# Kernel tuning notes

Measured on AMD Instinct MI355X. Metric: run time of the kernel, lower is better.

The kernel has to match this reference:

```python
import jax, jax.numpy as jnp
import numpy as np

N = 50000
E = 1600000
IN_C, H1, H2 = 512, 512, 256
N_CLASSES = 40
CENTER_NUM = 8
D_CAT = 2 * H2  # 512


def setup_inputs() -> dict:
    key = jax.random.key(0)
    ks = jax.random.split(key, 9)
    x = jax.random.normal(ks[0], (N, IN_C), dtype=jnp.float32)
    edge_index = jax.random.randint(ks[1], (2, E), 0, N, dtype=jnp.int64)
    s1 = 1.0 / np.sqrt(IN_C)
    s2 = 1.0 / np.sqrt(H1)
    sp = 1.0 / np.sqrt(D_CAT)
    W1 = jax.random.uniform(ks[2], (IN_C, H1), jnp.float32, -s1, s1)
    b1 = jnp.zeros((H1,), jnp.float32)
    W2 = jax.random.uniform(ks[3], (H1, H2), jnp.float32, -s2, s2)
    b2 = jnp.zeros((H2,), jnp.float32)
    Wp = jax.random.uniform(ks[4], (CENTER_NUM, D_CAT), jnp.float32, -sp, sp)   # interior_prototype weight [C, D]
    We = jax.random.uniform(ks[5], (CENTER_NUM, N_CLASSES, D_CAT), jnp.float32, -sp, sp)  # border prototypes
    return {"x": x, "edge_index": edge_index, "W1": W1, "b1": b1, "W2": W2, "b2": b2, "Wp": Wp, "We": We}


def _gcn_conv(x, W, b, src, dst, n):
    # PyG GCNConv: h = xW; out[i] = sum_j norm_ij h[j] + b, with self-loops,
    # norm_ij = deg_i^{-1/2} deg_j^{-1/2}, deg includes self-loop.
    h = x @ W
    ones = jnp.ones(src.shape[0], x.dtype)
    deg = jax.ops.segment_sum(ones, dst, num_segments=n) + 1.0
    dinv = deg ** -0.5
    norm = dinv[src] * dinv[dst]
    agg = jax.ops.segment_sum(h[src] * norm[:, None], dst, num_segments=n)
    agg = agg + h * (dinv * dinv)[:, None]  # self-loop term
    return agg + b


def _mean_aggr(x, src, dst, n):
    # PyG default message x_j with aggr='mean' (custom message_func kwarg is ignored by PyG)
    cnt = jax.ops.segment_sum(jnp.ones(src.shape[0], x.dtype), dst, num_segments=n)
    s = jax.ops.segment_sum(x[src], dst, num_segments=n)
    return s / jnp.maximum(cnt, 1.0)[:, None]


def reference(x, edge_index, W1, b1, W2, b2, Wp, We):
    src, dst = edge_index[0], edge_index[1]
    n = x.shape[0]
    h = jax.nn.relu(_gcn_conv(x, W1, b1, src, dst, n))
    h = _gcn_conv(h, W2, b2, src, dst, n)
    neighbor = _mean_aggr(h, src, dst, n)
    xc = jnp.concatenate([h, neighbor], axis=1)  # [N, 2*H2]
    scores = xc @ Wp.T                            # [N, C]
    idx = jnp.argmax(scores, axis=1)              # [N]
    # all-expert logits then per-node select (same math as masked per-cluster linear)
    all_out = jnp.einsum('nd,ckd->nck', xc, We)   # [N, C, n_classes]
    out = jnp.take_along_axis(all_out, idx[:, None, None], axis=1)[:, 0, :]
    return out, xc
```

## Files before the change

### kernel.cpp

```cpp
#include <hip/hip_runtime.h>
#include <hip/hip_bf16.h>
#include <hip/hip_fp16.h>
#include <cstdint>
#include <cstddef>


using short8 = __attribute__((ext_vector_type(8))) short;
using half8  = __attribute__((ext_vector_type(8))) _Float16;
using f32x4  = __attribute__((ext_vector_type(4))) float;

#define GLB_AS __attribute__((address_space(1)))
#define LDS_AS __attribute__((address_space(3)))

__device__ inline void unpack_fma(int v, float w, float* a) {
    a[0] = fmaf(w, (float)(char)(v),       a[0]);
    a[1] = fmaf(w, (float)(char)(v >> 8),  a[1]);
    a[2] = fmaf(w, (float)(char)(v >> 16), a[2]);
    a[3] = fmaf(w, (float)(v >> 24),       a[3]);
}

__global__ __launch_bounds__(256) void prep_kernel(
    const float* __restrict__ x, char* __restrict__ xq, float* __restrict__ scale,
    const float* __restrict__ W1, __half* __restrict__ W1T,
    const float* __restrict__ W2, __half* __restrict__ W2T,
    const float* __restrict__ We, __half* __restrict__ We_h,
    int* __restrict__ bcur, int* __restrict__ ecur,
    int n, int nbuck, int cap) {
    const int t = threadIdx.x;
    int b = blockIdx.x;
    const int BXQ = (n + 3) / 4;
    const int BW1 = (512 * 512) / 256;
    const int BW2 = (512 * 256) / 256;
    const int BWe = (8 * 40 * 512) / 256;
    if (b < BXQ) {
        const int node = b * 4 + (t >> 6);
        const int lane = t & 63;
        if (node < n) {
            const float* row = x + (size_t)node * 512;
            const float4 v0 = *(const float4*)&row[lane * 8];
            const float4 v1 = *(const float4*)&row[lane * 8 + 4];
            float m = fmaxf(fmaxf(fmaxf(fabsf(v0.x), fabsf(v0.y)), fmaxf(fabsf(v0.z), fabsf(v0.w))),
                            fmaxf(fmaxf(fabsf(v1.x), fabsf(v1.y)), fmaxf(fabsf(v1.z), fabsf(v1.w))));
#pragma unroll
            for (int off = 32; off; off >>= 1) m = fmaxf(m, __shfl_xor(m, off));
            m = fmaxf(m, 1e-30f);
            const float qs = 127.f / m;
            int q0 = __float2int_rn(v0.x * qs), q1 = __float2int_rn(v0.y * qs);
            int q2 = __float2int_rn(v0.z * qs), q3 = __float2int_rn(v0.w * qs);
            int q4 = __float2int_rn(v1.x * qs), q5 = __float2int_rn(v1.y * qs);
            int q6 = __float2int_rn(v1.z * qs), q7 = __float2int_rn(v1.w * qs);
            uint2 pk;
            pk.x = (q0 & 0xff) | ((q1 & 0xff) << 8) | ((q2 & 0xff) << 16) | ((q3 & 0xff) << 24);
            pk.y = (q4 & 0xff) | ((q5 & 0xff) << 8) | ((q6 & 0xff) << 16) | ((q7 & 0xff) << 24);
            *(uint2*)&xq[(size_t)node * 512 + lane * 8] = pk;
            if (lane == 0) scale[node] = m / 127.f;
        }
        return;
    }
    b -= BXQ;
    if (b < BW1) {
        const int gid = b * 256 + t;
        const int k = gid >> 9, nn = gid & 511;
        W1T[(size_t)nn * 512 + k] = __float2half(W1[gid]);
        return;
    }
    b -= BW1;
    if (b < BW2) {
        const int gid = b * 256 + t;
        const int k = gid >> 8, nn = gid & 255;
        W2T[(size_t)nn * 512 + k] = __float2half(W2[gid]);
        return;
    }
    b -= BW2;
    if (b < BWe) {
        const int gid = b * 256 + t;
        We_h[gid] = __float2half(We[gid]);
        return;
    }
    if (t < nbuck) bcur[t] = t * cap;
    if (t < 8) ecur[t] = 0;
}

__global__ __launch_bounds__(256) void bucketA_kernel(const int* __restrict__ src,
                                                      const int* __restrict__ dst,
                                                      int* __restrict__ bcur,
                                                      uint32_t* __restrict__ ebuf, int e) {
    __shared__ uint32_t sbuf[4096];
    __shared__ int h[128], gb[128], c2[128];
    const int t = threadIdx.x;
    if (t < 128) { h[t] = 0; c2[t] = 0; }
    __syncthreads();
    const int base = blockIdx.x * 4096;
    const int m = min(4096, e - base);
    for (int j = t; j < m; j += 256) {
        const int s = src[base + j];
        const int d = dst[base + j];
        sbuf[j] = ((uint32_t)s << 16) | (uint32_t)d;
        atomicAdd(&h[d >> 9], 1);
    }
    __syncthreads();
    if (t < 128 && h[t] > 0) gb[t] = atomicAdd(&bcur[t], h[t]);
    __syncthreads();
    for (int j = t; j < m; j += 256) {
        const uint32_t pf = sbuf[j];
        const int b = (int)((pf & 0xFFFFu) >> 9);
        const int r = atomicAdd(&c2[b], 1);
        ebuf[gb[b] + r] = pf;
    }
}

__global__ __launch_bounds__(256) void bucketB_kernel(const uint32_t* __restrict__ ebuf,
                                                      const int* __restrict__ bcur,
                                                      const float* __restrict__ scale,
                                                      int* __restrict__ offsets,
                                                      int* __restrict__ counts,
                                                      float* __restrict__ dinv,
                                                      float* __restrict__ dsc,
                                                      int* __restrict__ ssrc,
                                                      int n, int cap) {
    __shared__ int h[512];
    __shared__ int lofs[512];
    __shared__ int sc[256];
    const int t = threadIdx.x;
    const int b = blockIdx.x;
    const int nbase = b * 512;
    const int nb = min(512, n - nbase);
    h[t] = 0; h[t + 256] = 0;
    __syncthreads();
    const int ebeg = b * cap;
    const int ecount = bcur[b] - ebeg;
    for (int j = t; j < ecount; j += 256)
        atomicAdd(&h[ebuf[ebeg + j] & 511u], 1);
    __syncthreads();
    const int pair = h[2 * t] + h[2 * t + 1];
    sc[t] = pair;
    __syncthreads();
    for (int off = 1; off < 256; off <<= 1) {
        const int u = (t >= off) ? sc[t - off] : 0;
        __syncthreads();
        sc[t] += u;
        __syncthreads();
    }
    const int pbase = sc[t] - pair;
    lofs[2 * t] = pbase;
    lofs[2 * t + 1] = pbase + h[2 * t];
    __syncthreads();
    for (int j = t; j < nb; j += 256) {
        const int cnt = h[j];
        const float dv = rsqrtf((float)cnt + 1.0f);
        offsets[nbase + j] = ebeg + lofs[j];
        counts[nbase + j] = cnt;
        dinv[nbase + j] = dv;
        dsc[nbase + j] = dv * scale[nbase + j];
    }
    __syncthreads();
    lofs[2 * t] += ebeg;
    lofs[2 * t + 1] += ebeg;
    __syncthreads();
    for (int j = t; j < ecount; j += 256) {
        const uint32_t pf = ebuf[ebeg + j];
        const int d = (int)(pf & 511u);
        const int s = (int)(pf >> 16);
        const int pos = atomicAdd(&lofs[d], 1);
        ssrc[pos] = s;
    }
}

__global__ __launch_bounds__(256) void agg512_kernel(const char* __restrict__ xq,
                                                     const int* __restrict__ ssrc,
                                                     const int* __restrict__ offsets,
                                                     const int* __restrict__ counts,
                                                     const float* __restrict__ dinv,
                                                     const float* __restrict__ dsc,
                                                     __half* __restrict__ A16, int n) {
    const int lane = threadIdx.x & 63;
    const int node = (blockIdx.x * blockDim.x + threadIdx.x) >> 6;
    if (node >= n) return;
    const int beg = offsets[node];
    const int end = beg + counts[node];
    const float di = dinv[node];
    const int half = lane >> 5;
    const int hl = lane & 31;
    float acc[16];
#pragma unroll
    for (int j = 0; j < 16; ++j) acc[j] = 0.f;

    for (int b0 = beg; b0 < end; b0 += 64) {
        const int idx = b0 + lane;
        const int sl = (idx < end) ? ssrc[idx] : 0;
        const float wl = (idx < end) ? di * dsc[sl] : 0.f;
        const int m = min(64, end - b0);
#pragma unroll 8
        for (int kp = 0; kp < m; kp += 2) {
            const int k = kp + half;
            const int s = __shfl(sl, k);
            const float w = __shfl(wl, k);
            const int4 raw = *(const int4*)&xq[(size_t)s * 512 + hl * 16];
            unpack_fma(raw.x, w, &acc[0]);
            unpack_fma(raw.y, w, &acc[4]);
            unpack_fma(raw.z, w, &acc[8]);
            unpack_fma(raw.w, w, &acc[12]);
        }
    }
#pragma unroll
    for (int j = 0; j < 16; ++j) acc[j] += __shfl(acc[j], hl + 32);

    if (half == 0) {
        const float w = di * dsc[node];
        const int4 raw = *(const int4*)&xq[(size_t)node * 512 + hl * 16];
        unpack_fma(raw.x, w, &acc[0]);
        unpack_fma(raw.y, w, &acc[4]);
        unpack_fma(raw.z, w, &acc[8]);
        unpack_fma(raw.w, w, &acc[12]);
        float4 pk0, pk1;
        *(__half2*)&pk0.x = __floats2half2_rn(acc[0], acc[1]);
        *(__half2*)&pk0.y = __floats2half2_rn(acc[2], acc[3]);
        *(__half2*)&pk0.z = __floats2half2_rn(acc[4], acc[5]);
        *(__half2*)&pk0.w = __floats2half2_rn(acc[6], acc[7]);
        *(__half2*)&pk1.x = __floats2half2_rn(acc[8], acc[9]);
        *(__half2*)&pk1.y = __floats2half2_rn(acc[10], acc[11]);
        *(__half2*)&pk1.z = __floats2half2_rn(acc[12], acc[13]);
        *(__half2*)&pk1.w = __floats2half2_rn(acc[14], acc[15]);
        *(float4*)&A16[(size_t)node * 512 + hl * 16] = pk0;
        *(float4*)&A16[(size_t)node * 512 + hl * 16 + 8] = pk1;
    }
}

__global__ __launch_bounds__(256) void tquant_kernel(const __half* __restrict__ t16,
                                                     const float* __restrict__ dinv,
                                                     char* __restrict__ tq,
                                                     float* __restrict__ dts, int n) {
    const int lane = threadIdx.x & 63;
    const int node = (blockIdx.x * blockDim.x + threadIdx.x) >> 6;
    if (node >= n) return;
    const float2 raw = *(const float2*)&t16[(size_t)node * 256 + lane * 4];
    const float2 f0 = __half22float2(*(const __half2*)&raw.x);
    const float2 f1 = __half22float2(*(const __half2*)&raw.y);
    float m = fmaxf(fmaxf(fabsf(f0.x), fabsf(f0.y)), fmaxf(fabsf(f1.x), fabsf(f1.y)));
#pragma unroll
    for (int off = 32; off; off >>= 1) m = fmaxf(m, __shfl_xor(m, off));
    m = fmaxf(m, 1e-30f);
    const float qs = 127.f / m;
    const int q0 = __float2int_rn(f0.x * qs), q1 = __float2int_rn(f0.y * qs);
    const int q2 = __float2int_rn(f1.x * qs), q3 = __float2int_rn(f1.y * qs);
    const uint32_t pk = (q0 & 0xff) | ((q1 & 0xff) << 8) | ((q2 & 0xff) << 16) | ((q3 & 0xff) << 24);
    *(uint32_t*)&tq[(size_t)node * 256 + lane * 4] = pk;
    if (lane == 0) dts[node] = dinv[node] * (m / 127.f);
}

__global__ __launch_bounds__(256) void agg256_kernel(const char* __restrict__ tq,
                                                     const int* __restrict__ ssrc,
                                                     const int* __restrict__ offsets,
                                                     const int* __restrict__ counts,
                                                     const float* __restrict__ dinv,
                                                     const float* __restrict__ dts,
                                                     const float* __restrict__ bias,
                                                     float* __restrict__ xc,
                                                     __half* __restrict__ h2h,
                                                     char* __restrict__ hq8,
                                                     float* __restrict__ hsc, int n) {
    const int lane = threadIdx.x & 63;
    const int node = (blockIdx.x * blockDim.x + threadIdx.x) >> 6;
    if (node >= n) return;
    const int beg = offsets[node];
    const int end = beg + counts[node];
    const float di = dinv[node];
    const int q = lane >> 4;
    const int ql = lane & 15;
    float acc[16];
#pragma unroll
    for (int j = 0; j < 16; ++j) acc[j] = 0.f;

    for (int b0 = beg; b0 < end; b0 += 64) {
        const int idx = b0 + lane;
        const int sl = (idx < end) ? ssrc[idx] : 0;
        const float wl = (idx < end) ? di * dts[sl] : 0.f;
        const int m = min(64, end - b0);
#pragma unroll 4
        for (int kp = 0; kp < m; kp += 4) {
            const int k = kp + q;
            const int s = __shfl(sl, k);
            const float w = __shfl(wl, k);
            const int4 raw = *(const int4*)&tq[(size_t)s * 256 + ql * 16];
            unpack_fma(raw.x, w, &acc[0]);
            unpack_fma(raw.y, w, &acc[4]);
            unpack_fma(raw.z, w, &acc[8]);
            unpack_fma(raw.w, w, &acc[12]);
        }
    }
#pragma unroll
    for (int j = 0; j < 16; ++j) acc[j] += __shfl(acc[j], lane + 32);
#pragma unroll
    for (int j = 0; j < 16; ++j) acc[j] += __shfl(acc[j], lane + 16);

    if (q == 0) {
        const float w = di * dts[node];
        const int4 raw = *(const int4*)&tq[(size_t)node * 256 + ql * 16];
        unpack_fma(raw.x, w, &acc[0]);
        unpack_fma(raw.y, w, &acc[4]);
        unpack_fma(raw.z, w, &acc[8]);
        unpack_fma(raw.w, w, &acc[12]);
#pragma unroll
        for (int i = 0; i < 4; ++i) {
            const float4 bv = *(const float4*)&bias[ql * 16 + i * 4];
            acc[i * 4 + 0] += bv.x; acc[i * 4 + 1] += bv.y;
            acc[i * 4 + 2] += bv.z; acc[i * 4 + 3] += bv.w;
        }
#pragma unroll
        for (int i = 0; i < 4; ++i)
            *(float4*)&xc[(size_t)node * 512 + ql * 16 + i * 4] =
                make_float4(acc[i * 4 + 0], acc[i * 4 + 1], acc[i * 4 + 2], acc[i * 4 + 3]);
        float4 pk0, pk1;
        *(__half2*)&pk0.x = __floats2half2_rn(acc[0], acc[1]);
        *(__half2*)&pk0.y = __floats2half2_rn(acc[2], acc[3]);
        *(__half2*)&pk0.z = __floats2half2_rn(acc[4], acc[5]);
        *(__half2*)&pk0.w = __floats2half2_rn(acc[6], acc[7]);
        *(__half2*)&pk1.x = __floats2half2_rn(acc[8], acc[9]);
        *(__half2*)&pk1.y = __floats2half2_rn(acc[10], acc[11]);
        *(__half2*)&pk1.z = __floats2half2_rn(acc[12], acc[13]);
        *(__half2*)&pk1.w = __floats2half2_rn(acc[14], acc[15]);
        *(float4*)&h2h[(size_t)node * 256 + ql * 16] = pk0;
        *(float4*)&h2h[(size_t)node * 256 + ql * 16 + 8] = pk1;
        float am = 0.f;
#pragma unroll
        for (int j = 0; j < 16; ++j) am = fmaxf(am, fabsf(acc[j]));
#pragma unroll
        for (int off = 1; off < 16; off <<= 1) am = fmaxf(am, __shfl_xor(am, off));
        am = fmaxf(am, 1e-30f);
        const float qs = 127.f / am;
        uint32_t pk[4];
#pragma unroll
        for (int i = 0; i < 4; ++i) {
            const int a0 = __float2int_rn(acc[i * 4 + 0] * qs);
            const int a1 = __float2int_rn(acc[i * 4 + 1] * qs);
            const int a2 = __float2int_rn(acc[i * 4 + 2] * qs);
            const int a3 = __float2int_rn(acc[i * 4 + 3] * qs);
            pk[i] = (a0 & 0xff) | ((a1 & 0xff) << 8) | ((a2 & 0xff) << 16) | ((a3 & 0xff) << 24);
        }
        *(int4*)&hq8[(size_t)node * 256 + ql * 16] = *(int4*)pk;
        if (ql == 0) hsc[node] = am / 127.f;
    }
}

template <int EPI>
__global__ __launch_bounds__(256) void gemm_f16_kernel(
    const __half* __restrict__ A, const __half* __restrict__ WT,
    const float* __restrict__ bias, __half* __restrict__ C,
    int M, int N, int K, int ldc) {
    __shared__ ushort smem[2 * 4096];
    const int tid = threadIdx.x;
    const int lane = tid & 63;
    const int w = tid >> 6;
    const int wr = w >> 1, wc = w & 1;
    const int bm = blockIdx.y * 128;
    const int bn = blockIdx.x * 128;

    f32x4 acc[4][4];
#pragma unroll
    for (int i = 0; i < 4; ++i)
#pragma unroll
        for (int j = 0; j < 4; ++j) acc[i][j] = f32x4{0.f, 0.f, 0.f, 0.f};

    for (int k0 = 0; k0 < K; k0 += 32) {
        __syncthreads();
#pragma unroll
        for (int i = 0; i < 4; ++i) {
            const int q = w * 4 + i;
            const bool isA = q < 8;
            const int seg = (isA ? q : q - 8) * 64 + lane;
            const int row = seg >> 2;
            const int kc = (seg & 3) * 8;
            int grow = (isA ? bm : bn) + row;
            grow = min(grow, (isA ? M : N) - 1);
            const ushort* g = (const ushort*)(isA ? A : WT) + (size_t)grow * K + k0 + kc;
            __builtin_amdgcn_global_load_lds((const GLB_AS void*)g,
                                             (LDS_AS void*)(smem + q * 512), 16, 0, 0);
        }
        __syncthreads();

        const int koff = (lane >> 4) * 8;
        const int rsel = lane & 15;
        half8 a[4], b[4];
#pragma unroll
        for (int f = 0; f < 4; ++f) {
            const int ar = wr * 64 + f * 16 + rsel;
            a[f] = __builtin_bit_cast(half8, *(const short8*)&smem[ar * 32 + koff]);
            const int bc = wc * 64 + f * 16 + rsel;
            b[f] = __builtin_bit_cast(half8, *(const short8*)&smem[4096 + bc * 32 + koff]);
        }
#pragma unroll
        for (int i = 0; i < 4; ++i)
#pragma unroll
            for (int j = 0; j < 4; ++j)
                acc[i][j] = __builtin_amdgcn_mfma_f32_16x16x32_f16(a[i], b[j], acc[i][j], 0, 0, 0);
    }

    const int crow0 = wr * 64 + (lane >> 4) * 4;
    const int ccol0 = wc * 64 + (lane & 15);
#pragma unroll
    for (int f = 0; f < 4; ++f) {
#pragma unroll
        for (int g = 0; g < 4; ++g) {
            const int colg = bn + ccol0 + g * 16;
            float bv = 0.f;
            if constexpr (EPI == 1) bv = bias[colg];
#pragma unroll
            for (int j = 0; j < 4; ++j) {
                const int rowg = bm + crow0 + f * 16 + j;
                if (rowg >= M) continue;
                float v = acc[f][g][j];
                if constexpr (EPI == 1) v = fmaxf(v + bv, 0.f);
                C[(size_t)rowg * ldc + colg] = __float2half(v);
            }
        }
    }
}

__global__ __launch_bounds__(256) void mean_score_kernel(const int* __restrict__ ssrc,
                                                         const int* __restrict__ offsets,
                                                         const int* __restrict__ counts,
                                                         const float* __restrict__ Wp,
                                                         const char* __restrict__ hq8,
                                                         const float* __restrict__ hsc,
                                                         float* __restrict__ xc,
                                                         __half* __restrict__ mh,
                                                         int* __restrict__ bidx, int n) {
    __shared__ float lds_f[4][512];
    const int lane = threadIdx.x & 63;
    const int w = threadIdx.x >> 6;
    const int node = (blockIdx.x * blockDim.x + threadIdx.x) >> 6;
    if (node >= n) return;
    const int beg = offsets[node];
    const int cnt = counts[node];
    const int end = beg + cnt;
    const int c0 = lane * 4;
    const int q = lane >> 4;
    const int ql = lane & 15;

    float acc[16];
#pragma unroll
    for (int j = 0; j < 16; ++j) acc[j] = 0.f;
    for (int b0 = beg; b0 < end; b0 += 64) {
        const int idx = b0 + lane;
        const int sl = (idx < end) ? ssrc[idx] : 0;
        const float wl = (idx < end) ? hsc[sl] : 0.f;
        const int m = min(64, end - b0);
#pragma unroll 4
        for (int kp = 0; kp < m; kp += 4) {
            const int k = kp + q;
            const int s = __shfl(sl, k);
            const float ww = __shfl(wl, k);
            const int4 raw = *(const int4*)&hq8[(size_t)s * 256 + ql * 16];
            unpack_fma(raw.x, ww, &acc[0]);
            unpack_fma(raw.y, ww, &acc[4]);
            unpack_fma(raw.z, ww, &acc[8]);
            unpack_fma(raw.w, ww, &acc[12]);
        }
    }
#pragma unroll
    for (int j = 0; j < 16; ++j) acc[j] += __shfl(acc[j], lane + 32);
#pragma unroll
    for (int j = 0; j < 16; ++j) acc[j] += __shfl(acc[j], lane + 16);

    const float inv = 1.f / fmaxf((float)cnt, 1.f);
    if (q == 0) {
#pragma unroll
        for (int j = 0; j < 16; ++j) acc[j] *= inv;
#pragma unroll
        for (int i = 0; i < 4; ++i) {
            const float4 v = make_float4(acc[i * 4 + 0], acc[i * 4 + 1], acc[i * 4 + 2], acc[i * 4 + 3]);
            *(float4*)&xc[(size_t)node * 512 + 256 + ql * 16 + i * 4] = v;
            *(float4*)&lds_f[w][256 + ql * 16 + i * 4] = v;
        }
        float4 pk0, pk1;
        *(__half2*)&pk0.x = __floats2half2_rn(acc[0], acc[1]);
        *(__half2*)&pk0.y = __floats2half2_rn(acc[2], acc[3]);
        *(__half2*)&pk0.z = __floats2half2_rn(acc[4], acc[5]);
        *(__half2*)&pk0.w = __floats2half2_rn(acc[6], acc[7]);
        *(__half2*)&pk1.x = __floats2half2_rn(acc[8], acc[9]);
        *(__half2*)&pk1.y = __floats2half2_rn(acc[10], acc[11]);
        *(__half2*)&pk1.z = __floats2half2_rn(acc[12], acc[13]);
        *(__half2*)&pk1.w = __floats2half2_rn(acc[14], acc[15]);
        *(float4*)&mh[(size_t)node * 256 + ql * 16] = pk0;
        *(float4*)&mh[(size_t)node * 256 + ql * 16 + 8] = pk1;
    }
    const float4 a = *(const float4*)&xc[(size_t)node * 512 + c0];
    *(float4*)&lds_f[w][c0] = a;

    const int r = lane & 15;
    const int quad = lane >> 4;

    float av[32];
#pragma unroll
    for (int i = 0; i < 8; ++i) {
        const int jj = (i + r) & 7;
        *(float4*)&av[i * 4] = *(const float4*)&lds_f[w][r * 32 + jj * 4];
    }

    float s0, s1;
#pragma unroll
    for (int t = 0; t < 2; ++t) {
        const int c = t * 4 + quad;
        const float* wp = &Wp[c * 512 + r * 32];
        float p = 0.f;
#pragma unroll
        for (int i = 0; i < 8; ++i) {
            const int jj = (i + r) & 7;
            const float4 wv = *(const float4*)&wp[jj * 4];
            p = fmaf(av[i * 4 + 0], wv.x, p);
            p = fmaf(av[i * 4 + 1], wv.y, p);
            p = fmaf(av[i * 4 + 2], wv.z, p);
            p = fmaf(av[i * 4 + 3], wv.w, p);
        }
        p += __shfl_xor(p, 1); p += __shfl_xor(p, 2);
        p += __shfl_xor(p, 4); p += __shfl_xor(p, 8);
        if (t == 0) s0 = p; else s1 = p;
    }
    float best = -3.0e38f;
    int be = 0;
#pragma unroll
    for (int c = 0; c < 8; ++c) {
        const float v = __shfl((c < 4) ? s0 : s1, (c & 3) * 16);
        if (v > best) { best = v; be = c; }
    }
    if (lane == 0) bidx[node] = be;
}

__global__ __launch_bounds__(256) void bucket_scatter_kernel(const int* __restrict__ bidx,
                                                             int* __restrict__ cursor,
                                                             int* __restrict__ elist, int n) {
    __shared__ int h[8], base[8], c2[8];
    const int t = threadIdx.x;
    if (t < 8) { h[t] = 0; c2[t] = 0; }
    __syncthreads();
    const int i = blockIdx.x * 256 + t;
    int b = 0;
    if (i < n) {
        b = bidx[i];
        atomicAdd(&h[b], 1);
    }
    __syncthreads();
    if (t < 8) base[t] = (h[t] > 0) ? atomicAdd(&cursor[t], h[t]) : 0;
    __syncthreads();
    if (i < n) {
        const int r = atomicAdd(&c2[b], 1);
        elist[(size_t)b * n + base[b] + r] = i;
    }
}

__global__ __launch_bounds__(256) void expert_gemm_kernel(
    const int* __restrict__ elist, const int* __restrict__ ecnt,
    const __half* __restrict__ h2h, const __half* __restrict__ mh,
    const __half* __restrict__ We_h, float* __restrict__ out, int n) {
    const int e = blockIdx.x;
    const int cnt = ecnt[e];
    const int base = blockIdx.y * 128;
    if (base >= cnt) return;
    __shared__ __half Bs[40][520];
    const int tid = threadIdx.x;
#pragma unroll
    for (int i = 0; i < 10; ++i) {
        const int seg = tid + i * 256;
        const int br = seg >> 6;
        const int bc = (seg & 63) * 8;
        *(float4*)&Bs[br][bc] = *(const float4*)&We_h[((size_t)e * 40 + br) * 512 + bc];
    }
    __syncthreads();

    const int w = tid >> 6, lane = tid & 63;
    const int rsel = lane & 15, koff = (lane >> 4) * 8;
    const int grow0 = base + w * 32 + rsel;
    const int grow1 = grow0 + 16;
    const int i0 = elist[(size_t)e * n + min(grow0, cnt - 1)];
    const int i1 = elist[(size_t)e * n + min(grow1, cnt - 1)];

    f32x4 acc[2][3];
#pragma unroll
    for (int mf = 0; mf < 2; ++mf)
#pragma unroll
        for (int nf = 0; nf < 3; ++nf) acc[mf][nf] = f32x4{0.f, 0.f, 0.f, 0.f};

#pragma unroll
    for (int ks = 0; ks < 16; ++ks) {
        const int k0 = ks * 32 + koff;
        const __half* s0 = (k0 < 256) ? &h2h[(size_t)i0 * 256 + k0] : &mh[(size_t)i0 * 256 + (k0 - 256)];
        const __half* s1 = (k0 < 256) ? &h2h[(size_t)i1 * 256 + k0] : &mh[(size_t)i1 * 256 + (k0 - 256)];
        const half8 a0 = __builtin_bit_cast(half8, *(const short8*)s0);
        const half8 a1 = __builtin_bit_cast(half8, *(const short8*)s1);
#pragma unroll
        for (int nf = 0; nf < 3; ++nf) {
            const int brow = min(nf * 16 + rsel, 39);
            const half8 b = __builtin_bit_cast(half8, *(const short8*)&Bs[brow][ks * 32 + koff]);
            acc[0][nf] = __builtin_amdgcn_mfma_f32_16x16x32_f16(a0, b, acc[0][nf], 0, 0, 0);
            acc[1][nf] = __builtin_amdgcn_mfma_f32_16x16x32_f16(a1, b, acc[1][nf], 0, 0, 0);
        }
    }

    const int crow = (lane >> 4) * 4;
    const int ccol = lane & 15;
#pragma unroll
    for (int mf = 0; mf < 2; ++mf) {
#pragma unroll
        for (int nf = 0; nf < 3; ++nf) {
            const int col = nf * 16 + ccol;
            if (col >= 40) continue;
#pragma unroll
            for (int j = 0; j < 4; ++j) {
                const int gr = base + w * 32 + mf * 16 + crow + j;
                if (gr >= cnt) continue;
                const int node = elist[(size_t)e * n + gr];
                out[(size_t)node * 40 + col] = acc[mf][nf][j];
            }
        }
    }
}

extern "C" void kernel_launch(void* const* d_in, const int* in_sizes, int n_in,
                              void* d_out, int out_size, void* d_ws, size_t ws_size,
                              hipStream_t stream) {
    const float* x  = (const float*)d_in[0];
    const int*  edge = (const int*)d_in[1];
    const float* W1 = (const float*)d_in[2];
    const float* b1 = (const float*)d_in[3];
    const float* W2 = (const float*)d_in[4];
    const float* b2 = (const float*)d_in[5];
    const float* Wp = (const float*)d_in[6];
    const float* We = (const float*)d_in[7];

    const int n = in_sizes[0] / 512;
    const int e = in_sizes[1] / 2;
    const int* src = edge;
    const int* dst = edge + e;

    const int nbuck = (n + 511) / 512;
    const int cap = 20480;

    char* ws = (char*)d_ws;
    __half* A16 = (__half*)ws;
    __half* t16 = (__half*)ws;
    __half* mh  = (__half*)ws;
    char* p = ws + (size_t)n * 512 * 2;
    __half* h1 = (__half*)p;
    __half* h2h = (__half*)p;
    p += (size_t)n * 512 * 2;
    char* xq  = p; p += (size_t)n * 512;
    char* tq8 = p; p += (size_t)n * 256;
    char* hq8 = p; p += (size_t)n * 256;
    __half* W1T = (__half*)p; p += 512 * 512 * 2;
    __half* W2T = (__half*)p; p += 256 * 512 * 2;
    __half* We_h = (__half*)p; p += 8 * 40 * 512 * 2;
    auto align16 = [](size_t v) { return (v + 15) & ~(size_t)15; };
    float* scale = (float*)p;   p += align16((size_t)n * 4);
    float* dinv = (float*)p;    p += align16((size_t)n * 4);
    float* dsc = (float*)p;     p += align16((size_t)n * 4);
    float* dts = (float*)p;     p += align16((size_t)n * 4);
    float* hsc = (float*)p;     p += align16((size_t)n * 4);
    int* counts = (int*)p;      p += align16((size_t)n * 4);
    int* offsets = (int*)p;     p += align16((size_t)n * 4);
    int* bidx = (int*)p;        p += align16((size_t)n * 4);
    int* bcur = (int*)p;        p += align16((size_t)nbuck * 4);
    int* ecur = (int*)p;        p += align16((size_t)8 * 4);
    int* elist = (int*)p;       p += align16((size_t)8 * n * 4);
    uint32_t* ebuf = (uint32_t*)p; p += align16((size_t)nbuck * cap * 4);
    int* ssrc = (int*)p;

    float* out = (float*)d_out;
    float* xc = (float*)d_out + (size_t)n * 40;

    const int prep_blocks = (n + 3) / 4 + (512 * 512) / 256 +
                            (512 * 256) / 256 + (8 * 40 * 512) / 256 + 1;
    prep_kernel<<<prep_blocks, 256, 0, stream>>>(x, xq, scale, W1, W1T, W2, W2T, We, We_h,
                                                 bcur, ecur, n, nbuck, cap);

    bucketA_kernel<<<(e + 4095) / 4096, 256, 0, stream>>>(src, dst, bcur, ebuf, e);
    bucketB_kernel<<<nbuck, 256, 0, stream>>>(ebuf, bcur, scale, offsets, counts, dinv, dsc,
                                              ssrc, n, cap);

    const int waves_grid = (n * 64 + 255) / 256;
    agg512_kernel<<<waves_grid, 256, 0, stream>>>(xq, ssrc, offsets, counts, dinv, dsc, A16, n);
    dim3 g1(512 / 128, (n + 127) / 128);
    gemm_f16_kernel<1><<<g1, 256, 0, stream>>>(A16, W1T, b1, h1, n, 512, 512, 512);

    dim3 g2(256 / 128, (n + 127) / 128);
    gemm_f16_kernel<0><<<g2, 256, 0, stream>>>(h1, W2T, nullptr, t16, n, 256, 512, 256);
    tquant_kernel<<<waves_grid, 256, 0, stream>>>(t16, dinv, tq8, dts, n);

    agg256_kernel<<<waves_grid, 256, 0, stream>>>(tq8, ssrc, offsets, counts, dinv, dts, b2,
                                                  xc, h2h, hq8, hsc, n);

    mean_score_kernel<<<waves_grid, 256, 0, stream>>>(ssrc, offsets, counts, Wp, hq8, hsc,
                                                      xc, mh, bidx, n);

    bucket_scatter_kernel<<<(n + 255) / 256, 256, 0, stream>>>(bidx, ecur, elist, n);

    dim3 ge(8, (n + 127) / 128);
    expert_gemm_kernel<<<ge, 256, 0, stream>>>(elist, ecur, h2h, mh, We_h, out, n);
}
```

Before: 557.9 us.

## Switch int8 activations to offset-uint8 and feed the expert GEMM from 8-bit data

```diff
diff --git a/kernel.cpp b/kernel.cpp
--- a/kernel.cpp
+++ b/kernel.cpp
@@ -8,19 +8,34 @@
 using short8 = __attribute__((ext_vector_type(8))) short;
 using half8  = __attribute__((ext_vector_type(8))) _Float16;
 using f32x4  = __attribute__((ext_vector_type(4))) float;
+typedef unsigned char uchar;
 
 #define GLB_AS __attribute__((address_space(1)))
 #define LDS_AS __attribute__((address_space(3)))
 
-__device__ inline void unpack_fma(int v, float w, float* a) {
-    a[0] = fmaf(w, (float)(char)(v),       a[0]);
-    a[1] = fmaf(w, (float)(char)(v >> 8),  a[1]);
-    a[2] = fmaf(w, (float)(char)(v >> 16), a[2]);
-    a[3] = fmaf(w, (float)(v >> 24),       a[3]);
+__device__ inline void unpack_fma_u(uint32_t v, float w, float* a) {
+    a[0] = fmaf(w, (float)(v & 0xffu),         a[0]);
+    a[1] = fmaf(w, (float)((v >> 8) & 0xffu),  a[1]);
+    a[2] = fmaf(w, (float)((v >> 16) & 0xffu), a[2]);
+    a[3] = fmaf(w, (float)(v >> 24),           a[3]);
+}
+
+__device__ inline half8 dequant8(uint2 raw, float s) {
+    const float off = -128.f * s;
+    half8 r;
+    r[0] = (_Float16)fmaf(s, (float)(raw.x & 0xffu), off);
+    r[1] = (_Float16)fmaf(s, (float)((raw.x >> 8) & 0xffu), off);
+    r[2] = (_Float16)fmaf(s, (float)((raw.x >> 16) & 0xffu), off);
+    r[3] = (_Float16)fmaf(s, (float)(raw.x >> 24), off);
+    r[4] = (_Float16)fmaf(s, (float)(raw.y & 0xffu), off);
+    r[5] = (_Float16)fmaf(s, (float)((raw.y >> 8) & 0xffu), off);
+    r[6] = (_Float16)fmaf(s, (float)((raw.y >> 16) & 0xffu), off);
+    r[7] = (_Float16)fmaf(s, (float)(raw.y >> 24), off);
+    return r;
 }
 
 __global__ __launch_bounds__(256) void prep_kernel(
-    const float* __restrict__ x, char* __restrict__ xq, float* __restrict__ scale,
+    const float* __restrict__ x, uchar* __restrict__ xq, float* __restrict__ scale,
     const float* __restrict__ W1, __half* __restrict__ W1T,
     const float* __restrict__ W2, __half* __restrict__ W2T,
     const float* __restrict__ We, __half* __restrict__ We_h,
@@ -45,13 +60,13 @@
             for (int off = 32; off; off >>= 1) m = fmaxf(m, __shfl_xor(m, off));
             m = fmaxf(m, 1e-30f);
             const float qs = 127.f / m;
-            int q0 = __float2int_rn(v0.x * qs), q1 = __float2int_rn(v0.y * qs);
-            int q2 = __float2int_rn(v0.z * qs), q3 = __float2int_rn(v0.w * qs);
-            int q4 = __float2int_rn(v1.x * qs), q5 = __float2int_rn(v1.y * qs);
-            int q6 = __float2int_rn(v1.z * qs), q7 = __float2int_rn(v1.w * qs);
+            const int q0 = __float2int_rn(v0.x * qs) + 128, q1 = __float2int_rn(v0.y * qs) + 128;
+            const int q2 = __float2int_rn(v0.z * qs) + 128, q3 = __float2int_rn(v0.w * qs) + 128;
+            const int q4 = __float2int_rn(v1.x * qs) + 128, q5 = __float2int_rn(v1.y * qs) + 128;
+            const int q6 = __float2int_rn(v1.z * qs) + 128, q7 = __float2int_rn(v1.w * qs) + 128;
             uint2 pk;
-            pk.x = (q0 & 0xff) | ((q1 & 0xff) << 8) | ((q2 & 0xff) << 16) | ((q3 & 0xff) << 24);
-            pk.y = (q4 & 0xff) | ((q5 & 0xff) << 8) | ((q6 & 0xff) << 16) | ((q7 & 0xff) << 24);
+            pk.x = q0 | (q1 << 8) | (q2 << 16) | (q3 << 24);
+            pk.y = q4 | (q5 << 8) | (q6 << 16) | (q7 << 24);
             *(uint2*)&xq[(size_t)node * 512 + lane * 8] = pk;
             if (lane == 0) scale[node] = m / 127.f;
         }
@@ -166,7 +181,7 @@
     }
 }
 
-__global__ __launch_bounds__(256) void agg512_kernel(const char* __restrict__ xq,
+__global__ __launch_bounds__(256) void agg512_kernel(const uchar* __restrict__ xq,
                                                      const int* __restrict__ ssrc,
                                                      const int* __restrict__ offsets,
                                                      const int* __restrict__ counts,
@@ -184,6 +199,7 @@
     float acc[16];
 #pragma unroll
     for (int j = 0; j < 16; ++j) acc[j] = 0.f;
+    float wsum = 0.f;
 
     for (int b0 = beg; b0 < end; b0 += 64) {
         const int idx = b0 + lane;
@@ -195,23 +211,28 @@
             const int k = kp + half;
             const int s = __shfl(sl, k);
             const float w = __shfl(wl, k);
-            const int4 raw = *(const int4*)&xq[(size_t)s * 512 + hl * 16];
-            unpack_fma(raw.x, w, &acc[0]);
-            unpack_fma(raw.y, w, &acc[4]);
-            unpack_fma(raw.z, w, &acc[8]);
-            unpack_fma(raw.w, w, &acc[12]);
+            wsum += w;
+            const uint4 raw = *(const uint4*)&xq[(size_t)s * 512 + hl * 16];
+            unpack_fma_u(raw.x, w, &acc[0]);
+            unpack_fma_u(raw.y, w, &acc[4]);
+            unpack_fma_u(raw.z, w, &acc[8]);
+            unpack_fma_u(raw.w, w, &acc[12]);
         }
     }
 #pragma unroll
     for (int j = 0; j < 16; ++j) acc[j] += __shfl(acc[j], hl + 32);
+    wsum += __shfl(wsum, hl + 32);
 
     if (half == 0) {
         const float w = di * dsc[node];
-        const int4 raw = *(const int4*)&xq[(size_t)node * 512 + hl * 16];
-        unpack_fma(raw.x, w, &acc[0]);
-        unpack_fma(raw.y, w, &acc[4]);
-        unpack_fma(raw.z, w, &acc[8]);
-        unpack_fma(raw.w, w, &acc[12]);
+        wsum += w;
+        const uint4 raw = *(const uint4*)&xq[(size_t)node * 512 + hl * 16];
+        unpack_fma_u(raw.x, w, &acc[0]);
+        unpack_fma_u(raw.y, w, &acc[4]);
+        unpack_fma_u(raw.z, w, &acc[8]);
+        unpack_fma_u(raw.w, w, &acc[12]);
+#pragma unroll
+        for (int j = 0; j < 16; ++j) acc[j] = fmaf(-128.f, wsum, acc[j]);
         float4 pk0, pk1;
         *(__half2*)&pk0.x = __floats2half2_rn(acc[0], acc[1]);
         *(__half2*)&pk0.y = __floats2half2_rn(acc[2], acc[3]);
@@ -228,7 +249,7 @@
 
 __global__ __launch_bounds__(256) void tquant_kernel(const __half* __restrict__ t16,
                                                      const float* __restrict__ dinv,
-                                                     char* __restrict__ tq,
+                                                     uchar* __restrict__ tq,
                                                      float* __restrict__ dts, int n) {
     const int lane = threadIdx.x & 63;
     const int node = (blockIdx.x * blockDim.x + threadIdx.x) >> 6;
@@ -241,14 +262,14 @@
     for (int off = 32; off; off >>= 1) m = fmaxf(m, __shfl_xor(m, off));
     m = fmaxf(m, 1e-30f);
     const float qs = 127.f / m;
-    const int q0 = __float2int_rn(f0.x * qs), q1 = __float2int_rn(f0.y * qs);
-    const int q2 = __float2int_rn(f1.x * qs), q3 = __float2int_rn(f1.y * qs);
-    const uint32_t pk = (q0 & 0xff) | ((q1 & 0xff) << 8) | ((q2 & 0xff) << 16) | ((q3 & 0xff) << 24);
+    const int q0 = __float2int_rn(f0.x * qs) + 128, q1 = __float2int_rn(f0.y * qs) + 128;
+    const int q2 = __float2int_rn(f1.x * qs) + 128, q3 = __float2int_rn(f1.y * qs) + 128;
+    const uint32_t pk = q0 | (q1 << 8) | (q2 << 16) | (q3 << 24);
     *(uint32_t*)&tq[(size_t)node * 256 + lane * 4] = pk;
     if (lane == 0) dts[node] = dinv[node] * (m / 127.f);
 }
 
-__global__ __launch_bounds__(256) void agg256_kernel(const char* __restrict__ tq,
+__global__ __launch_bounds__(256) void agg256_kernel(const uchar* __restrict__ tq,
                                                      const int* __restrict__ ssrc,
                                                      const int* __restrict__ offsets,
                                                      const int* __restrict__ counts,
@@ -256,8 +277,7 @@
                                                      const float* __restrict__ dts,
                                                      const float* __restrict__ bias,
                                                      float* __restrict__ xc,
-                                                     __half* __restrict__ h2h,
-                                                     char* __restrict__ hq8,
+                                                     uchar* __restrict__ hq8,
                                                      float* __restrict__ hsc, int n) {
     const int lane = threadIdx.x & 63;
     const int node = (blockIdx.x * blockDim.x + threadIdx.x) >> 6;
@@ -270,6 +290,7 @@
     float acc[16];
 #pragma unroll
     for (int j = 0; j < 16; ++j) acc[j] = 0.f;
+    float wsum = 0.f;
 
     for (int b0 = beg; b0 < end; b0 += 64) {
         const int idx = b0 + lane;
@@ -281,25 +302,31 @@
             const int k = kp + q;
             const int s = __shfl(sl, k);
             const float w = __shfl(wl, k);
-            const int4 raw = *(const int4*)&tq[(size_t)s * 256 + ql * 16];
-            unpack_fma(raw.x, w, &acc[0]);
-            unpack_fma(raw.y, w, &acc[4]);
-            unpack_fma(raw.z, w, &acc[8]);
-            unpack_fma(raw.w, w, &acc[12]);
+            wsum += w;
+            const uint4 raw = *(const uint4*)&tq[(size_t)s * 256 + ql * 16];
+            unpack_fma_u(raw.x, w, &acc[0]);
+            unpack_fma_u(raw.y, w, &acc[4]);
+            unpack_fma_u(raw.z, w, &acc[8]);
+            unpack_fma_u(raw.w, w, &acc[12]);
         }
     }
 #pragma unroll
     for (int j = 0; j < 16; ++j) acc[j] += __shfl(acc[j], lane + 32);
+    wsum += __shfl(wsum, lane + 32);
 #pragma unroll
     for (int j = 0; j < 16; ++j) acc[j] += __shfl(acc[j], lane + 16);
+    wsum += __shfl(wsum, lane + 16);
 
     if (q == 0) {
         const float w = di * dts[node];
-        const int4 raw = *(const int4*)&tq[(size_t)node * 256 + ql * 16];
-        unpack_fma(raw.x, w, &acc[0]);
-        unpack_fma(raw.y, w, &acc[4]);
-        unpack_fma(raw.z, w, &acc[8]);
-        unpack_fma(raw.w, w, &acc[12]);
+        wsum += w;
+        const uint4 raw = *(const uint4*)&tq[(size_t)node * 256 + ql * 16];
+        unpack_fma_u(raw.x, w, &acc[0]);
+        unpack_fma_u(raw.y, w, &acc[4]);
+        unpack_fma_u(raw.z, w, &acc[8]);
+        unpack_fma_u(raw.w, w, &acc[12]);
+#pragma unroll
+        for (int j = 0; j < 16; ++j) acc[j] = fmaf(-128.f, wsum, acc[j]);
 #pragma unroll
         for (int i = 0; i < 4; ++i) {
             const float4 bv = *(const float4*)&bias[ql * 16 + i * 4];
@@ -310,17 +337,6 @@
         for (int i = 0; i < 4; ++i)
             *(float4*)&xc[(size_t)node * 512 + ql * 16 + i * 4] =
                 make_float4(acc[i * 4 + 0], acc[i * 4 + 1], acc[i * 4 + 2], acc[i * 4 + 3]);
-        float4 pk0, pk1;
-        *(__half2*)&pk0.x = __floats2half2_rn(acc[0], acc[1]);
-        *(__half2*)&pk0.y = __floats2half2_rn(acc[2], acc[3]);
-        *(__half2*)&pk0.z = __floats2half2_rn(acc[4], acc[5]);
-        *(__half2*)&pk0.w = __floats2half2_rn(acc[6], acc[7]);
-        *(__half2*)&pk1.x = __floats2half2_rn(acc[8], acc[9]);
-        *(__half2*)&pk1.y = __floats2half2_rn(acc[10], acc[11]);
-        *(__half2*)&pk1.z = __floats2half2_rn(acc[12], acc[13]);
-        *(__half2*)&pk1.w = __floats2half2_rn(acc[14], acc[15]);
-        *(float4*)&h2h[(size_t)node * 256 + ql * 16] = pk0;
-        *(float4*)&h2h[(size_t)node * 256 + ql * 16 + 8] = pk1;
         float am = 0.f;
 #pragma unroll
         for (int j = 0; j < 16; ++j) am = fmaxf(am, fabsf(acc[j]));
@@ -331,13 +347,13 @@
         uint32_t pk[4];
 #pragma unroll
         for (int i = 0; i < 4; ++i) {
-            const int a0 = __float2int_rn(acc[i * 4 + 0] * qs);
-            const int a1 = __float2int_rn(acc[i * 4 + 1] * qs);
-            const int a2 = __float2int_rn(acc[i * 4 + 2] * qs);
-            const int a3 = __float2int_rn(acc[i * 4 + 3] * qs);
-            pk[i] = (a0 & 0xff) | ((a1 & 0xff) << 8) | ((a2 & 0xff) << 16) | ((a3 & 0xff) << 24);
-        }
-        *(int4*)&hq8[(size_t)node * 256 + ql * 16] = *(int4*)pk;
+            const int a0 = __float2int_rn(acc[i * 4 + 0] * qs) + 128;
+            const int a1 = __float2int_rn(acc[i * 4 + 1] * qs) + 128;
+            const int a2 = __float2int_rn(acc[i * 4 + 2] * qs) + 128;
+            const int a3 = __float2int_rn(acc[i * 4 + 3] * qs) + 128;
+            pk[i] = a0 | (a1 << 8) | (a2 << 16) | (a3 << 24);
+        }
+        *(uint4*)&hq8[(size_t)node * 256 + ql * 16] = *(uint4*)pk;
         if (ql == 0) hsc[node] = am / 127.f;
     }
 }
@@ -420,10 +436,11 @@
                                                          const int* __restrict__ offsets,
                                                          const int* __restrict__ counts,
                                                          const float* __restrict__ Wp,
-                                                         const char* __restrict__ hq8,
+                                                         const uchar* __restrict__ hq8,
                                                          const float* __restrict__ hsc,
                                                          float* __restrict__ xc,
-                                                         __half* __restrict__ mh,
+                                                         uchar* __restrict__ mq8,
+                                                         float* __restrict__ msc,
                                                          int* __restrict__ bidx, int n) {
     __shared__ float lds_f[4][512];
     const int lane = threadIdx.x & 63;
@@ -440,6 +457,7 @@
     float acc[16];
 #pragma unroll
     for (int j = 0; j < 16; ++j) acc[j] = 0.f;
+    float wsum = 0.f;
     for (int b0 = beg; b0 < end; b0 += 64) {
         const int idx = b0 + lane;
         const int sl = (idx < end) ? ssrc[idx] : 0;
@@ -450,39 +468,49 @@
             const int k = kp + q;
             const int s = __shfl(sl, k);
             const float ww = __shfl(wl, k);
-            const int4 raw = *(const int4*)&hq8[(size_t)s * 256 + ql * 16];
-            unpack_fma(raw.x, ww, &acc[0]);
-            unpack_fma(raw.y, ww, &acc[4]);
-            unpack_fma(raw.z, ww, &acc[8]);
-            unpack_fma(raw.w, ww, &acc[12]);
+            wsum += ww;
+            const uint4 raw = *(const uint4*)&hq8[(size_t)s * 256 + ql * 16];
+            unpack_fma_u(raw.x, ww, &acc[0]);
+            unpack_fma_u(raw.y, ww, &acc[4]);
+            unpack_fma_u(raw.z, ww, &acc[8]);
+            unpack_fma_u(raw.w, ww, &acc[12]);
         }
     }
 #pragma unroll
     for (int j = 0; j < 16; ++j) acc[j] += __shfl(acc[j], lane + 32);
+    wsum += __shfl(wsum, lane + 32);
 #pragma unroll
     for (int j = 0; j < 16; ++j) acc[j] += __shfl(acc[j], lane + 16);
+    wsum += __shfl(wsum, lane + 16);
 
     const float inv = 1.f / fmaxf((float)cnt, 1.f);
     if (q == 0) {
 #pragma unroll
-        for (int j = 0; j < 16; ++j) acc[j] *= inv;
+        for (int j = 0; j < 16; ++j) acc[j] = fmaf(-128.f, wsum, acc[j]) * inv;
 #pragma unroll
         for (int i = 0; i < 4; ++i) {
             const float4 v = make_float4(acc[i * 4 + 0], acc[i * 4 + 1], acc[i * 4 + 2], acc[i * 4 + 3]);
             *(float4*)&xc[(size_t)node * 512 + 256 + ql * 16 + i * 4] = v;
             *(float4*)&lds_f[w][256 + ql * 16 + i * 4] = v;
         }
-        float4 pk0, pk1;
-        *(__half2*)&pk0.x = __floats2half2_rn(acc[0], acc[1]);
-        *(__half2*)&pk0.y = __floats2half2_rn(acc[2], acc[3]);
-        *(__half2*)&pk0.z = __floats2half2_rn(acc[4], acc[5]);
-        *(__half2*)&pk0.w = __floats2half2_rn(acc[6], acc[7]);
-        *(__half2*)&pk1.x = __floats2half2_rn(acc[8], acc[9]);
-        *(__half2*)&pk1.y = __floats2half2_rn(acc[10], acc[11]);
-        *(__half2*)&pk1.z = __floats2half2_rn(acc[12], acc[13]);
-        *(__half2*)&pk1.w = __floats2half2_rn(acc[14], acc[15]);
-        *(float4*)&mh[(size_t)node * 256 + ql * 16] = pk0;
-        *(float4*)&mh[(size_t)node * 256 + ql * 16 + 8] = pk1;
+        float am = 0.f;
+#pragma unroll
+        for (int j = 0; j < 16; ++j) am = fmaxf(am, fabsf(acc[j]));
+#pragma unroll
+        for (int off = 1; off < 16; off <<= 1) am = fmaxf(am, __shfl_xor(am, off));
+        am = fmaxf(am, 1e-30f);
+        const float qs = 127.f / am;
+        uint32_t pk[4];
+#pragma unroll
+        for (int i = 0; i < 4; ++i) {
+            const int a0 = __float2int_rn(acc[i * 4 + 0] * qs) + 128;
+            const int a1 = __float2int_rn(acc[i * 4 + 1] * qs) + 128;
+            const int a2 = __float2int_rn(acc[i * 4 + 2] * qs) + 128;
+            const int a3 = __float2int_rn(acc[i * 4 + 3] * qs) + 128;
+            pk[i] = a0 | (a1 << 8) | (a2 << 16) | (a3 << 24);
+        }
+        *(uint4*)&mq8[(size_t)node * 256 + ql * 16] = *(uint4*)pk;
+        if (ql == 0) msc[node] = am / 127.f;
     }
     const float4 a = *(const float4*)&xc[(size_t)node * 512 + c0];
     *(float4*)&lds_f[w][c0] = a;
@@ -550,7 +578,8 @@
 
 __global__ __launch_bounds__(256) void expert_gemm_kernel(
     const int* __restrict__ elist, const int* __restrict__ ecnt,
-    const __half* __restrict__ h2h, const __half* __restrict__ mh,
+    const uchar* __restrict__ hq8, const float* __restrict__ hsc,
+    const uchar* __restrict__ mq8, const float* __restrict__ msc,
     const __half* __restrict__ We_h, float* __restrict__ out, int n) {
     const int e = blockIdx.x;
     const int cnt = ecnt[e];
@@ -573,6 +602,8 @@
     const int grow1 = grow0 + 16;
     const int i0 = elist[(size_t)e * n + min(grow0, cnt - 1)];
     const int i1 = elist[(size_t)e * n + min(grow1, cnt - 1)];
+    const float hs0 = hsc[i0], ms0 = msc[i0];
+    const float hs1 = hsc[i1], ms1 = msc[i1];
 
     f32x4 acc[2][3];
 #pragma unroll
@@ -583,10 +614,11 @@
 #pragma unroll
     for (int ks = 0; ks < 16; ++ks) {
         const int k0 = ks * 32 + koff;
-        const __half* s0 = (k0 < 256) ? &h2h[(size_t)i0 * 256 + k0] : &mh[(size_t)i0 * 256 + (k0 - 256)];
-        const __half* s1 = (k0 < 256) ? &h2h[(size_t)i1 * 256 + k0] : &mh[(size_t)i1 * 256 + (k0 - 256)];
-        const half8 a0 = __builtin_bit_cast(half8, *(const short8*)s0);
-        const half8 a1 = __builtin_bit_cast(half8, *(const short8*)s1);
+        const bool lo = ks < 8;
+        const uchar* p0 = lo ? &hq8[(size_t)i0 * 256 + k0] : &mq8[(size_t)i0 * 256 + (k0 - 256)];
+        const uchar* p1 = lo ? &hq8[(size_t)i1 * 256 + k0] : &mq8[(size_t)i1 * 256 + (k0 - 256)];
+        const half8 a0 = dequant8(*(const uint2*)p0, lo ? hs0 : ms0);
+        const half8 a1 = dequant8(*(const uint2*)p1, lo ? hs1 : ms1);
 #pragma unroll
         for (int nf = 0; nf < 3; ++nf) {
             const int brow = min(nf * 16 + rsel, 39);
@@ -638,14 +670,13 @@
     char* ws = (char*)d_ws;
     __half* A16 = (__half*)ws;
     __half* t16 = (__half*)ws;
-    __half* mh  = (__half*)ws;
+    uchar*  mq8 = (uchar*)ws;
     char* p = ws + (size_t)n * 512 * 2;
     __half* h1 = (__half*)p;
-    __half* h2h = (__half*)p;
+    uchar* tq8 = (uchar*)p;
+    uchar* hq8 = (uchar*)p + (size_t)n * 256;
     p += (size_t)n * 512 * 2;
-    char* xq  = p; p += (size_t)n * 512;
-    char* tq8 = p; p += (size_t)n * 256;
-    char* hq8 = p; p += (size_t)n * 256;
+    uchar* xq = (uchar*)p; p += (size_t)n * 512;
     __half* W1T = (__half*)p; p += 512 * 512 * 2;
     __half* W2T = (__half*)p; p += 256 * 512 * 2;
     __half* We_h = (__half*)p; p += 8 * 40 * 512 * 2;
@@ -655,6 +686,7 @@
     float* dsc = (float*)p;     p += align16((size_t)n * 4);
     float* dts = (float*)p;     p += align16((size_t)n * 4);
     float* hsc = (float*)p;     p += align16((size_t)n * 4);
+    float* msc = (float*)p;     p += align16((size_t)n * 4);
     int* counts = (int*)p;      p += align16((size_t)n * 4);
     int* offsets = (int*)p;     p += align16((size_t)n * 4);
     int* bidx = (int*)p;        p += align16((size_t)n * 4);
@@ -686,13 +718,13 @@
     tquant_kernel<<<waves_grid, 256, 0, stream>>>(t16, dinv, tq8, dts, n);
 
     agg256_kernel<<<waves_grid, 256, 0, stream>>>(tq8, ssrc, offsets, counts, dinv, dts, b2,
-                                                  xc, h2h, hq8, hsc, n);
+                                                  xc, hq8, hsc, n);
 
     mean_score_kernel<<<waves_grid, 256, 0, stream>>>(ssrc, offsets, counts, Wp, hq8, hsc,
-                                                      xc, mh, bidx, n);
+                                                      xc, mq8, msc, bidx, n);
 
     bucket_scatter_kernel<<<(n + 255) / 256, 256, 0, stream>>>(bidx, ecur, elist, n);
 
     dim3 ge(8, (n + 127) / 128);
-    expert_gemm_kernel<<<ge, 256, 0, stream>>>(elist, ecur, h2h, mh, We_h, out, n);
-}
+    expert_gemm_kernel<<<ge, 256, 0, stream>>>(elist, ecur, hq8, hsc, mq8, msc, We_h, out, n);
+}
```

Result: no change. 551.3 us (-1.2%).
